# Optimization experiments

Measured on AMD Instinct MI355X. Metric: run time of the kernel, lower is better.

## Reference

```python
import jax, jax.numpy as jnp
import numpy as np

B, L, K, H = 2, 2048, 48, 128
NUM_IN = 2 * H          # h_E (H) + gathered h_V (H)
SCALE = 30.0            # EncLayer scale
LN_EPS = 1e-5


def _linear_params(key, fan_in, fan_out):
    kw, kb = jax.random.split(key)
    s = 1.0 / np.sqrt(fan_in)
    W = jax.random.uniform(kw, (fan_in, fan_out), minval=-s, maxval=s, dtype=jnp.float32)
    b = jax.random.uniform(kb, (fan_out,), minval=-s, maxval=s, dtype=jnp.float32)
    return W, b


def setup_inputs() -> dict:
    key = jax.random.key(0)
    ks = jax.random.split(key, 12)
    h_V = jax.random.normal(ks[0], (B, L, H), dtype=jnp.float32)
    h_E = jax.random.normal(ks[1], (B, L, K, H), dtype=jnp.float32)
    E_idx = jax.random.randint(ks[2], (B, L, K), 0, L, dtype=jnp.int64)
    mask_V = jnp.ones((B, L), dtype=jnp.float32)
    mask_attend = jnp.ones((B, L, K), dtype=jnp.float32)

    W1, b1 = _linear_params(ks[3], H + NUM_IN, H)
    W2, b2 = _linear_params(ks[4], H, H)
    W3, b3 = _linear_params(ks[5], H, H)
    W11, b11 = _linear_params(ks[6], H + NUM_IN, H)
    W12, b12 = _linear_params(ks[7], H, H)
    W13, b13 = _linear_params(ks[8], H, H)
    Wi, bi = _linear_params(ks[9], H, 4 * H)   # PositionWiseFeedForward W_in
    Wo, bo = _linear_params(ks[10], 4 * H, H)  # W_out

    ln = lambda: (jnp.ones((H,), jnp.float32), jnp.zeros((H,), jnp.float32))
    ln1_s, ln1_b = ln(); ln2_s, ln2_b = ln(); ln3_s, ln3_b = ln()

    return dict(h_V=h_V, h_E=h_E, E_idx=E_idx, mask_V=mask_V, mask_attend=mask_attend,
                W1=W1, b1=b1, W2=W2, b2=b2, W3=W3, b3=b3,
                W11=W11, b11=b11, W12=W12, b12=b12, W13=W13, b13=b13,
                Wi=Wi, bi=bi, Wo=Wo, bo=bo,
                ln1_s=ln1_s, ln1_b=ln1_b, ln2_s=ln2_s, ln2_b=ln2_b,
                ln3_s=ln3_s, ln3_b=ln3_b)


def gather_nodes(nodes, idx):
    # nodes: [B, L, H], idx: [B, L, K] -> [B, L, K, H]
    b, l, h = nodes.shape
    flat = idx.reshape(b, -1)  # [B, L*K]
    g = jnp.take_along_axis(nodes, flat[..., None], axis=1)  # [B, L*K, H]
    return g.reshape(b, idx.shape[1], idx.shape[2], h)


def layer_norm(x, scale, bias):
    mu = jnp.mean(x, axis=-1, keepdims=True)
    var = jnp.mean((x - mu) ** 2, axis=-1, keepdims=True)
    return (x - mu) / jnp.sqrt(var + LN_EPS) * scale + bias


def gelu(x):
    return jax.nn.gelu(x, approximate=False)  # torch nn.GELU default (erf)


def enc_layer_forward(h_V, h_E, E_idx, mask_V, mask_attend, p):
    # --- node update: gather neighbors, concat, MLP, masked sum-reduce ---
    h_EV = jnp.concatenate([h_E, gather_nodes(h_V, E_idx)], axis=-1)        # [B,L,K,2H]
    h_V_exp = jnp.broadcast_to(h_V[:, :, None, :], h_EV.shape[:3] + (h_V.shape[-1],))
    h_EV = jnp.concatenate([h_V_exp, h_EV], axis=-1)                        # [B,L,K,3H]
    m = gelu(h_EV @ p['W1'] + p['b1'])
    m = gelu(m @ p['W2'] + p['b2'])
    m = m @ p['W3'] + p['b3']
    m = mask_attend[..., None] * m
    dh = jnp.sum(m, axis=-2) / SCALE                                        # [B,L,H]
    h_V = layer_norm(h_V + dh, p['ln1_s'], p['ln1_b'])
    # --- position-wise FFN ---
    dh = gelu(h_V @ p['Wi'] + p['bi']) @ p['Wo'] + p['bo']
    h_V = layer_norm(h_V + dh, p['ln2_s'], p['ln2_b'])
    h_V = mask_V[..., None] * h_V
    # --- edge update ---
    h_EV = jnp.concatenate([h_E, gather_nodes(h_V, E_idx)], axis=-1)
    h_V_exp = jnp.broadcast_to(h_V[:, :, None, :], h_EV.shape[:3] + (h_V.shape[-1],))
    h_EV = jnp.concatenate([h_V_exp, h_EV], axis=-1)
    m = gelu(h_EV @ p['W11'] + p['b11'])
    m = gelu(m @ p['W12'] + p['b12'])
    m = m @ p['W13'] + p['b13']
    h_E = layer_norm(h_E + m, p['ln3_s'], p['ln3_b'])
    return h_V, h_E


def reference(h_V, h_E, E_idx, mask_V, mask_attend,
              W1, b1, W2, b2, W3, b3, W11, b11, W12, b12, W13, b13,
              Wi, bi, Wo, bo, ln1_s, ln1_b, ln2_s, ln2_b, ln3_s, ln3_b):
    p = dict(W1=W1, b1=b1, W2=W2, b2=b2, W3=W3, b3=b3,
             W11=W11, b11=b11, W12=W12, b12=b12, W13=W13, b13=b13,
             Wi=Wi, bi=bi, Wo=Wo, bo=bo,
             ln1_s=ln1_s, ln1_b=ln1_b, ln2_s=ln2_s, ln2_b=ln2_b,
             ln3_s=ln3_s, ln3_b=ln3_b)
    return enc_layer_forward(h_V, h_E, E_idx, mask_V, mask_attend, p)
```

## Files before the change

kernel.cpp:

```cpp
#include <hip/hip_runtime.h>
#include <hip/hip_bf16.h>
#include <math.h>

typedef unsigned short u16;
typedef __attribute__((ext_vector_type(8))) short bf16x8;
typedef __attribute__((ext_vector_type(4))) float f32x4;
typedef __attribute__((ext_vector_type(4))) unsigned int uint4v;

#define BB 2
#define LL 2048
#define KN 48
#define HH 128
#define NBLK (BB*LL)
#define ST 136

#define WOFF      16
#define OFF_W1MT  (WOFF + 0)
#define OFF_W1ST  (WOFF + 16384)
#define OFF_W1GT  (WOFF + 32768)
#define OFF_W2T   (WOFF + 49152)
#define OFF_W3T   (WOFF + 65536)
#define OFF_W11MT (WOFF + 81920)
#define OFF_W11ST (WOFF + 98304)
#define OFF_W11GT (WOFF + 114688)
#define OFF_W12T  (WOFF + 131072)
#define OFF_W13T  (WOFF + 147456)
#define OFF_WIT   (WOFF + 163840)
#define OFF_WOT   (WOFF + 229376)
#define OFF_HV1   (WOFF + 294912)
#define OFF_Q1    (WOFF + 819200)
#define OFF_Q2    (WOFF + 1343488)
#define OFF_R1    (WOFF + 1867776)
#define OFF_R2    (WOFF + 2916352)
#define PREP_N    294912

__device__ __forceinline__ float b2f(u16 u){
    union { unsigned int i; float f; } v; v.i = ((unsigned int)u) << 16; return v.f;
}
__device__ __forceinline__ u16 f2b(float f){
    unsigned int x = __float_as_uint(f);
    unsigned int r = x + 0x7fffu + ((x >> 16) & 1u);
    return (u16)(r >> 16);
}
__device__ __forceinline__ unsigned int f2b2(float lo, float hi){
    unsigned int r;
    asm("v_cvt_pk_bf16_f32 %0, %1, %2" : "=v"(r) : "v"(lo), "v"(hi));
    return r;
}
__device__ __forceinline__ float gelu_f(float x){
    float ax = fabsf(x) * 0.70710678118654752f;
    float t  = __builtin_amdgcn_rcpf(fmaf(0.3275911f, ax, 1.0f));
    float e  = __builtin_amdgcn_exp2f(ax * ax * -1.4426950408889634f);
    float p  = fmaf(1.061405429f, t, -1.453152027f);
    p = fmaf(p, t, 1.421413741f);
    p = fmaf(p, t, -0.284496736f);
    p = fmaf(p, t, 0.254829592f);
    p = p * t;
    float erfv = fmaf(-p, e, 1.0f);
    float hx = 0.5f * x;
    return fmaf(fabsf(hx), erfv, hx);
}
__device__ __forceinline__ u16 ldb(const void* p, long i, int f32){
    return f32 ? f2b(((const float*)p)[i]) : ((const u16*)p)[i];
}
__device__ __forceinline__ float ldf(const void* p, long i, int f32){
    return f32 ? ((const float*)p)[i] : b2f(((const u16*)p)[i]);
}
__device__ __forceinline__ void stage8(u16* dst, const void* src, long off, int f32){
    if (f32){
        const float* s = (const float*)src + off;
        unsigned int r0 = f2b2(s[0], s[1]);
        unsigned int r1 = f2b2(s[2], s[3]);
        unsigned int r2 = f2b2(s[4], s[5]);
        unsigned int r3 = f2b2(s[6], s[7]);
        uint4v v; v.x = r0; v.y = r1; v.z = r2; v.w = r3;
        *(uint4v*)dst = v;
    } else {
        *(uint4v*)dst = *(const uint4v*)((const u16*)src + off);
    }
}
__device__ __forceinline__ int ld_idx(const void* p, int i, int i64){
    int v = i64 ? ((const int*)p)[2*i] : ((const int*)p)[i];
    return v & (LL - 1);
}
__device__ __forceinline__ void st_out(void* p, long i, float v, int f32){
    if (f32) ((float*)p)[i] = v;
    else ((u16*)p)[i] = f2b(v);
}

__global__ void detect_kernel(const void* ln1s, const void* maskV, const void* eidx, int* flags){
    if (threadIdx.x == 0){
        unsigned l0 = ((const unsigned*)ln1s)[0];
        unsigned m0 = ((const unsigned*)maskV)[0];
        int f32 = (l0 == 0x3F800000u || m0 == 0x3F800000u) ? 1 : 0;
        const int* e = (const int*)eidx;
        int orodd = 0, orlow = 0;
        for (int i = 1; i < 64; i += 2) orodd |= e[i];
        for (int i = 0; i < 64; i += 2) orlow |= e[i];
        flags[0] = f32;
        flags[1] = (orodd == 0 && orlow != 0) ? 1 : 0;
    }
}

__global__ void prep_kernel(const void* W1, const void* W2, const void* W3,
                            const void* W11, const void* W12, const void* W13,
                            const void* Wi, const void* Wo, u16* wsbase){
    const int f32 = ((const int*)wsbase)[0];
    int i = blockIdx.x * 256 + threadIdx.x;
    if (i < 16384){ int n = i >> 7, k = i & 127; wsbase[OFF_W1MT + i] = ldb(W1, (128 + k)*128 + n, f32); }
    else if (i < 32768){ int j = i - 16384;  int n = j >> 7, k = j & 127; wsbase[OFF_W1ST  + j] = ldb(W1, k*128 + n, f32); }
    else if (i < 49152){ int j = i - 32768;  int n = j >> 7, k = j & 127; wsbase[OFF_W1GT  + j] = ldb(W1, (256 + k)*128 + n, f32); }
    else if (i < 65536){ int j = i - 49152;  int n = j >> 7, k = j & 127; wsbase[OFF_W2T   + j] = ldb(W2, k*128 + n, f32); }
    else if (i < 81920){ int j = i - 65536;  int n = j >> 7, k = j & 127; wsbase[OFF_W3T   + j] = ldb(W3, k*128 + n, f32); }
    else if (i < 98304){ int j = i - 81920;  int n = j >> 7, k = j & 127; wsbase[OFF_W11MT + j] = ldb(W11, (128 + k)*128 + n, f32); }
    else if (i < 114688){ int j = i - 98304; int n = j >> 7, k = j & 127; wsbase[OFF_W11ST + j] = ldb(W11, k*128 + n, f32); }
    else if (i < 131072){ int j = i - 114688;int n = j >> 7, k = j & 127; wsbase[OFF_W11GT + j] = ldb(W11, (256 + k)*128 + n, f32); }
    else if (i < 147456){ int j = i - 131072;int n = j >> 7, k = j & 127; wsbase[OFF_W12T  + j] = ldb(W12, k*128 + n, f32); }
    else if (i < 163840){ int j = i - 147456;int n = j >> 7, k = j & 127; wsbase[OFF_W13T  + j] = ldb(W13, k*128 + n, f32); }
    else if (i < 229376){ int j = i - 163840; int h = j >> 7, c = j & 127; wsbase[OFF_WIT + j] = ldb(Wi, c*512 + h, f32); }
    else if (i < 294912){ int j = i - 229376; int c = j >> 9, h = j & 511; wsbase[OFF_WOT + j] = ldb(Wo, h*128 + c, f32); }
}

__global__ __launch_bounds__(256) void precomp_kernel(
    const void* __restrict__ src, const void* __restrict__ bias,
    u16* __restrict__ wsbase, long offWs, long offWg, long offQ, long offR)
{
    __shared__ alignas(16) u16 X[16 * ST];
    const int f32 = ((const int*)wsbase)[0];
    const int t = threadIdx.x, lane = t & 63, w = t >> 6;
    const int node0 = blockIdx.x * 16;
    const int r16 = lane & 15, q = lane >> 4, q8 = q * 8;

    {
        int row = t >> 4, ch = t & 15;
        stage8(X + row * ST + ch * 8, src, ((long)(node0 + row)) * HH + ch * 8, f32);
    }
    __syncthreads();

    bf16x8 a[4];
    {
        const u16* ap = X + r16 * ST + q8;
#pragma unroll
        for (int kk = 0; kk < 4; kk++) a[kk] = *(const bf16x8*)(ap + kk * 32);
    }
#pragma unroll
    for (int half = 0; half < 2; half++){
        long offW = half ? offWg : offWs;
#pragma unroll
        for (int nt = 0; nt < 2; nt++){
            int col = w * 32 + nt * 16 + r16;
            const u16* bp = wsbase + offW + (long)col * 128 + q8;
            f32x4 acc; acc[0]=0.f; acc[1]=0.f; acc[2]=0.f; acc[3]=0.f;
#pragma unroll
            for (int kk = 0; kk < 4; kk++){
                bf16x8 bv = *(const bf16x8*)(bp + kk * 32);
                acc = __builtin_amdgcn_mfma_f32_16x16x32_bf16(a[kk], bv, acc, 0, 0, 0);
            }
            if (half == 0){
                float* Rf = (float*)(wsbase + offR);
                float bc = ldf(bias, col, f32);
#pragma unroll
                for (int i = 0; i < 4; i++){
                    int row = q * 4 + i;
                    Rf[(long)(node0 + row) * HH + col] = acc[i] + bc;
                }
            } else {
#pragma unroll
                for (int i = 0; i < 4; i++){
                    int row = q * 4 + i;
                    wsbase[offQ + (long)(node0 + row) * HH + col] = f2b(acc[i]);
                }
            }
        }
    }
}

__device__ __forceinline__ void mfma_regB(const u16* Als, const bf16x8* B,
                                          f32x4 acc[3], int lane){
    const int r16 = lane & 15;
    const int q8  = (lane >> 4) * 8;
    const u16* ap = Als + r16 * ST + q8;
#pragma unroll
    for (int kk = 0; kk < 4; kk++){
        bf16x8 a0 = *(const bf16x8*)(ap + kk * 32);
        bf16x8 a1 = *(const bf16x8*)(ap + 16 * ST + kk * 32);
        bf16x8 a2 = *(const bf16x8*)(ap + 32 * ST + kk * 32);
        acc[0] = __builtin_amdgcn_mfma_f32_16x16x32_bf16(a0, B[kk], acc[0], 0, 0, 0);
        acc[1] = __builtin_amdgcn_mfma_f32_16x16x32_bf16(a1, B[kk], acc[1], 0, 0, 0);
        acc[2] = __builtin_amdgcn_mfma_f32_16x16x32_bf16(a2, B[kk], acc[2], 0, 0, 0);
    }
}

__device__ __forceinline__ void zero_acc3(f32x4 acc[3]){
#pragma unroll
    for (int m = 0; m < 3; m++){ acc[m][0]=0.f; acc[m][1]=0.f; acc[m][2]=0.f; acc[m][3]=0.f; }
}

__device__ __forceinline__ void init_acc3(f32x4 acc[3], const u16* Qg, int lane, int w){
    const int r16 = lane & 15, q = lane >> 4;
    const int col = w * 16 + r16;
#pragma unroll
    for (int mt = 0; mt < 3; mt++)
#pragma unroll
        for (int i = 0; i < 4; i++){
            int r = mt * 16 + q * 4 + i;
            acc[mt][i] = b2f(Qg[r * ST + col]);
        }
}

__device__ __forceinline__ void store_m8(f32x4 acc[3], u16* M, float bc,
                                         int lane, int w, bool dogelu){
    const int r16 = lane & 15, q = lane >> 4;
    int col = w * 16 + r16;
#pragma unroll
    for (int mt = 0; mt < 3; mt++){
        float v0 = acc[mt][0] + bc, v1 = acc[mt][1] + bc;
        float v2 = acc[mt][2] + bc, v3 = acc[mt][3] + bc;
        if (dogelu){ v0 = gelu_f(v0); v1 = gelu_f(v1); v2 = gelu_f(v2); v3 = gelu_f(v3); }
        unsigned int p0 = f2b2(v0, v1), p1 = f2b2(v2, v3);
        int r = mt * 16 + q * 4;
        M[(r + 0) * ST + col] = (u16)p0;
        M[(r + 1) * ST + col] = (u16)(p0 >> 16);
        M[(r + 2) * ST + col] = (u16)p1;
        M[(r + 3) * ST + col] = (u16)(p1 >> 16);
    }
}

__global__ __launch_bounds__(512, 6) void node_kernel(
    const void* __restrict__ hV, const void* __restrict__ hE, const void* __restrict__ Eidx,
    const void* __restrict__ maskA,
    const void* __restrict__ b2, const void* __restrict__ b3,
    const void* __restrict__ ln1s, const void* __restrict__ ln1b,
    u16* __restrict__ wsbase)
{
    __shared__ alignas(16) u16 A[KN * ST];
    __shared__ alignas(16) u16 Qg[KN * ST];
    __shared__ alignas(16) u16 M1[KN * ST];
    __shared__ float smask[KN];
    __shared__ float dh[HH];
    __shared__ float hv0f[HH];
    u16* M2 = A;

    const int f32 = ((const int*)wsbase)[0];
    const int i64 = ((const int*)wsbase)[1];
    const u16* ws = wsbase;
    const int t = threadIdx.x, lane = t & 63, w = t >> 6;
    const int bid = blockIdx.x;
    const int b = bid >> 11;
    const int r16 = lane & 15, q8 = (lane >> 4) * 8;
    const int col = w * 16 + r16;

    bf16x8 B1[4];
    {
        const u16* bp = ws + OFF_W1MT + (long)col * 128 + q8;
#pragma unroll
        for (int k = 0; k < 4; k++) B1[k] = *(const bf16x8*)(bp + k * 32);
    }

    for (int i = t; i < 768; i += 512){
        int row = i >> 4, ch = i & 15;
        stage8(A + row * ST + ch * 8, hE, ((long)bid * KN + row) * HH + ch * 8, f32);
    }
    for (int i = t; i < 768; i += 512){
        int row = i >> 4, ch = i & 15;
        int nb = ld_idx(Eidx, bid * KN + row, i64);
        *(uint4v*)(Qg + row * ST + ch * 8) =
            *(const uint4v*)(ws + OFF_Q1 + ((long)b * LL + nb) * HH + ch * 8);
    }
    if (t < HH) hv0f[t] = ldf(hV, (long)bid * HH + t, f32);
    if (t < KN) smask[t] = ldf(maskA, bid * KN + t, f32);

    bf16x8 B2[4];
    {
        const u16* bp = ws + OFF_W2T + (long)col * 128 + q8;
#pragma unroll
        for (int k = 0; k < 4; k++) B2[k] = *(const bf16x8*)(bp + k * 32);
    }
    const float bcf = ((const float*)(wsbase + OFF_R1))[(long)bid * HH + col];
    __syncthreads();

    f32x4 acc[3];
    init_acc3(acc, Qg, lane, w);
    mfma_regB(A, B1, acc, lane);
    store_m8(acc, M1, bcf, lane, w, true);

    bf16x8 B3[4];
    {
        const u16* bp = ws + OFF_W3T + (long)col * 128 + q8;
#pragma unroll
        for (int k = 0; k < 4; k++) B3[k] = *(const bf16x8*)(bp + k * 32);
    }
    __syncthreads();

    zero_acc3(acc);
    mfma_regB(M1, B2, acc, lane);
    store_m8(acc, M2, ldf(b2, col, f32), lane, w, true);
    __syncthreads();

    zero_acc3(acc);
    mfma_regB(M2, B3, acc, lane);

    {
        const int q = lane >> 4;
        float bc = ldf(b3, col, f32);
        float s0 = 0.f;
#pragma unroll
        for (int mt = 0; mt < 3; mt++)
#pragma unroll
            for (int i = 0; i < 4; i++){
                int r = mt * 16 + q * 4 + i;
                s0 += smask[r] * (acc[mt][i] + bc);
            }
        s0 += __shfl_xor(s0, 16); s0 += __shfl_xor(s0, 32);
        if (lane < 16) dh[w * 16 + lane] = s0;
    }
    __syncthreads();

    if (w == 0){
        float xa = hv0f[lane]      + dh[lane]      * (1.0f / 30.0f);
        float xb = hv0f[64 + lane] + dh[64 + lane] * (1.0f / 30.0f);
        float sum = xa + xb, sq = xa * xa + xb * xb;
#pragma unroll
        for (int off = 1; off < 64; off <<= 1){ sum += __shfl_xor(sum, off); sq += __shfl_xor(sq, off); }
        float mu = sum * (1.0f / 128.0f);
        float var = sq * (1.0f / 128.0f) - mu * mu;
        float rstd = rsqrtf(var + 1e-5f);
        wsbase[OFF_HV1 + (long)bid * HH + lane] =
            f2b((xa - mu) * rstd * ldf(ln1s, lane, f32) + ldf(ln1b, lane, f32));
        wsbase[OFF_HV1 + (long)bid * HH + 64 + lane] =
            f2b((xb - mu) * rstd * ldf(ln1s, 64 + lane, f32) + ldf(ln1b, 64 + lane, f32));
    }
}

__global__ __launch_bounds__(512, 6) void ffn_kernel(
    const void* __restrict__ maskV,
    const void* __restrict__ bi, const void* __restrict__ bo,
    const void* __restrict__ ln2s, const void* __restrict__ ln2b,
    u16* __restrict__ wsbase, void* __restrict__ dout)
{
    __shared__ alignas(16) u16 X[16 * 136];
    __shared__ alignas(16) u16 Hid[16 * 520];
    __shared__ float V[16 * 132];

    const int f32 = ((const int*)wsbase)[0];
    const u16* ws = wsbase;
    const u16* hv1 = wsbase + OFF_HV1;
    const int t = threadIdx.x, lane = t & 63, w = t >> 6;
    const int node0 = blockIdx.x * 16;
    const int r16 = lane & 15, q = lane >> 4, q8 = q * 8;

    if (t < 256){
        int row = t >> 4, ch = t & 15;
        *(uint4v*)(X + row * 136 + ch * 8) =
            *(const uint4v*)(hv1 + (long)(node0 + row) * HH + ch * 8);
    }
    __syncthreads();

    bf16x8 a[4];
    {
        const u16* ap = X + r16 * 136 + q8;
#pragma unroll
        for (int kk = 0; kk < 4; kk++) a[kk] = *(const bf16x8*)(ap + kk * 32);
    }
    f32x4 acc[4];
#pragma unroll
    for (int nt = 0; nt < 4; nt++){
        acc[nt][0]=0.f; acc[nt][1]=0.f; acc[nt][2]=0.f; acc[nt][3]=0.f;
        int n = w * 64 + nt * 16 + r16;
        const u16* bp = ws + OFF_WIT + (long)n * 128 + q8;
#pragma unroll
        for (int kk = 0; kk < 4; kk++){
            bf16x8 bv = *(const bf16x8*)(bp + kk * 32);
            acc[nt] = __builtin_amdgcn_mfma_f32_16x16x32_bf16(a[kk], bv, acc[nt], 0, 0, 0);
        }
    }
#pragma unroll
    for (int nt = 0; nt < 4; nt++){
        int col = w * 64 + nt * 16 + r16;
        float bc = ldf(bi, col, f32);
        float g0 = gelu_f(acc[nt][0] + bc), g1 = gelu_f(acc[nt][1] + bc);
        float g2 = gelu_f(acc[nt][2] + bc), g3 = gelu_f(acc[nt][3] + bc);
        unsigned int p0 = f2b2(g0, g1), p1 = f2b2(g2, g3);
        int row = q * 4;
        Hid[(row + 0) * 520 + col] = (u16)p0;
        Hid[(row + 1) * 520 + col] = (u16)(p0 >> 16);
        Hid[(row + 2) * 520 + col] = (u16)p1;
        Hid[(row + 3) * 520 + col] = (u16)(p1 >> 16);
    }
    __syncthreads();

    f32x4 acc2; acc2[0]=0.f; acc2[1]=0.f; acc2[2]=0.f; acc2[3]=0.f;
    {
        const u16* ap = Hid + r16 * 520 + q8;
        const u16* bp = ws + OFF_WOT + (long)(w * 16 + r16) * 512 + q8;
#pragma unroll
        for (int kk = 0; kk < 16; kk++){
            bf16x8 av = *(const bf16x8*)(ap + kk * 32);
            bf16x8 bv = *(const bf16x8*)(bp + kk * 32);
            acc2 = __builtin_amdgcn_mfma_f32_16x16x32_bf16(av, bv, acc2, 0, 0, 0);
        }
    }
    {
        int col = w * 16 + r16;
        float bc = ldf(bo, col, f32);
#pragma unroll
        for (int i = 0; i < 4; i++){
            int row = q * 4 + i;
            V[row * 132 + col] = acc2[i] + bc + b2f(X[row * 136 + col]);
        }
    }
    __syncthreads();

    {
        int row = t >> 5, p = t & 31;
        float v0 = V[row * 132 + p * 4 + 0];
        float v1 = V[row * 132 + p * 4 + 1];
        float v2 = V[row * 132 + p * 4 + 2];
        float v3 = V[row * 132 + p * 4 + 3];
        float sum = v0 + v1 + v2 + v3;
        float sq = v0*v0 + v1*v1 + v2*v2 + v3*v3;
#pragma unroll
        for (int off = 1; off < 32; off <<= 1){ sum += __shfl_xor(sum, off); sq += __shfl_xor(sq, off); }
        float mu = sum * (1.0f / 128.0f);
        float var = sq * (1.0f / 128.0f) - mu * mu;
        float rstd = rsqrtf(var + 1e-5f);
        float mv = ldf(maskV, node0 + row, f32);
        long base = (long)(node0 + row) * HH;
#pragma unroll
        for (int j = 0; j < 4; j++){
            int c = p * 4 + j;
            float v = (j==0)?v0:(j==1)?v1:(j==2)?v2:v3;
            float y = ((v - mu) * rstd * ldf(ln2s, c, f32) + ldf(ln2b, c, f32)) * mv;
            st_out(dout, base + c, y, f32);
        }
    }
}

__global__ __launch_bounds__(512, 6) void edge_kernel(
    const void* __restrict__ hE, const void* __restrict__ Eidx,
    const void* __restrict__ b12, const void* __restrict__ b13,
    const void* __restrict__ ln3s, const void* __restrict__ ln3b,
    u16* __restrict__ wsbase, void* __restrict__ dout)
{
    __shared__ alignas(16) u16 A[KN * ST];
    __shared__ alignas(16) u16 Qg[KN * ST];
    __shared__ alignas(16) u16 M1[KN * ST];
    __shared__ float rowsum[KN];
    __shared__ float rowsq[KN];
    u16* M2 = A;

    const int f32 = ((const int*)wsbase)[0];
    const int i64 = ((const int*)wsbase)[1];
    const u16* ws = wsbase;
    const int t = threadIdx.x, lane = t & 63, w = t >> 6;
    const int bid = blockIdx.x;
    const int b = bid >> 11;
    const int r16 = lane & 15, q8 = (lane >> 4) * 8;
    const int col = w * 16 + r16;

    bf16x8 B1[4];
    {
        const u16* bp = ws + OFF_W11MT + (long)col * 128 + q8;
#pragma unroll
        for (int k = 0; k < 4; k++) B1[k] = *(const bf16x8*)(bp + k * 32);
    }

    for (int i = t; i < 768; i += 512){
        int row = i >> 4, ch = i & 15;
        stage8(A + row * ST + ch * 8, hE, ((long)bid * KN + row) * HH + ch * 8, f32);
    }
    for (int i = t; i < 768; i += 512){
        int row = i >> 4, ch = i & 15;
        int nb = ld_idx(Eidx, bid * KN + row, i64);
        *(uint4v*)(Qg + row * ST + ch * 8) =
            *(const uint4v*)(ws + OFF_Q2 + ((long)b * LL + nb) * HH + ch * 8);
    }
    if (t < KN){ rowsum[t] = 0.f; rowsq[t] = 0.f; }

    bf16x8 B2[4];
    {
        const u16* bp = ws + OFF_W12T + (long)col * 128 + q8;
#pragma unroll
        for (int k = 0; k < 4; k++) B2[k] = *(const bf16x8*)(bp + k * 32);
    }
    const float bcf = ((const float*)(wsbase + OFF_R2))[(long)bid * HH + col];
    __syncthreads();

    f32x4 acc[3];
    init_acc3(acc, Qg, lane, w);
    mfma_regB(A, B1, acc, lane);
    store_m8(acc, M1, bcf, lane, w, true);

    bf16x8 B3[4];
    {
        const u16* bp = ws + OFF_W13T + (long)col * 128 + q8;
#pragma unroll
        for (int k = 0; k < 4; k++) B3[k] = *(const bf16x8*)(bp + k * 32);
    }
    __syncthreads();

    zero_acc3(acc);
    mfma_regB(M1, B2, acc, lane);
    store_m8(acc, M2, ldf(b12, col, f32), lane, w, true);
    __syncthreads();

    zero_acc3(acc);
    mfma_regB(M2, B3, acc, lane);

    const int q = lane >> 4;
    float vals[3][4];
    {
        float bc = ldf(b13, col, f32);
#pragma unroll
        for (int mt = 0; mt < 3; mt++)
#pragma unroll
            for (int i = 0; i < 4; i++){
                int r = mt * 16 + q * 4 + i;
                vals[mt][i] = acc[mt][i] + bc + ldf(hE, ((long)bid * KN + r) * HH + col, f32);
            }
    }
#pragma unroll
    for (int mt = 0; mt < 3; mt++)
#pragma unroll
        for (int i = 0; i < 4; i++){
            float s = vals[mt][i], sq2 = vals[mt][i] * vals[mt][i];
            s += __shfl_xor(s, 1); sq2 += __shfl_xor(sq2, 1);
            s += __shfl_xor(s, 2); sq2 += __shfl_xor(sq2, 2);
            s += __shfl_xor(s, 4); sq2 += __shfl_xor(sq2, 4);
            s += __shfl_xor(s, 8); sq2 += __shfl_xor(sq2, 8);
            if (r16 == 0){
                int r = mt * 16 + q * 4 + i;
                atomicAdd(&rowsum[r], s);
                atomicAdd(&rowsq[r], sq2);
            }
        }
    __syncthreads();
    if (t < KN){
        float mu = rowsum[t] * (1.0f / 128.0f);
        float var = rowsq[t] * (1.0f / 128.0f) - mu * mu;
        rowsum[t] = mu;
        rowsq[t] = rsqrtf(var + 1e-5f);
    }
    __syncthreads();

    {
        long ebase = (long)BB * LL * HH;
        float g = ldf(ln3s, col, f32), be = ldf(ln3b, col, f32);
#pragma unroll
        for (int mt = 0; mt < 3; mt++)
#pragma unroll
            for (int i = 0; i < 4; i++){
                int r = mt * 16 + q * 4 + i;
                long base = ebase + ((long)bid * KN + r) * HH;
                st_out(dout, base + col, (vals[mt][i] - rowsum[r]) * rowsq[r] * g + be, f32);
            }
    }
}

extern "C" void kernel_launch(void* const* d_in, const int* in_sizes, int n_in,
                              void* d_out, int out_size, void* d_ws, size_t ws_size,
                              hipStream_t stream) {
    const void* hV    = d_in[0];
    const void* hE    = d_in[1];
    const void* Eidx  = d_in[2];
    const void* maskV = d_in[3];
    const void* maskA = d_in[4];
    const void* W1  = d_in[5];  const void* b1  = d_in[6];
    const void* W2  = d_in[7];  const void* b2  = d_in[8];
    const void* W3  = d_in[9];  const void* b3  = d_in[10];
    const void* W11 = d_in[11]; const void* b11 = d_in[12];
    const void* W12 = d_in[13]; const void* b12 = d_in[14];
    const void* W13 = d_in[15]; const void* b13 = d_in[16];
    const void* Wi  = d_in[17]; const void* bi  = d_in[18];
    const void* Wo  = d_in[19]; const void* bo  = d_in[20];
    const void* ln1s = d_in[21]; const void* ln1b = d_in[22];
    const void* ln2s = d_in[23]; const void* ln2b = d_in[24];
    const void* ln3s = d_in[25]; const void* ln3b = d_in[26];

    u16* ws = (u16*)d_ws;

    detect_kernel<<<1, 64, 0, stream>>>(ln1s, maskV, Eidx, (int*)d_ws);
    prep_kernel<<<(PREP_N + 255) / 256, 256, 0, stream>>>(W1, W2, W3, W11, W12, W13, Wi, Wo, ws);
    precomp_kernel<<<NBLK / 16, 256, 0, stream>>>(hV, b1, ws,
                                                  (long)OFF_W1ST, (long)OFF_W1GT,
                                                  (long)OFF_Q1, (long)OFF_R1);
    node_kernel<<<NBLK, 512, 0, stream>>>(hV, hE, Eidx, maskA,
                                          b2, b3, ln1s, ln1b, ws);
    ffn_kernel<<<NBLK / 16, 512, 0, stream>>>(maskV, bi, bo, ln2s, ln2b, ws, d_out);
    precomp_kernel<<<NBLK / 16, 256, 0, stream>>>(d_out, b11, ws,
                                                  (long)OFF_W11ST, (long)OFF_W11GT,
                                                  (long)OFF_Q2, (long)OFF_R2);
    edge_kernel<<<NBLK, 512, 0, stream>>>(hE, Eidx, b12, b13,
                                          ln3s, ln3b, ws, d_out);
}
```

Measured before the change: 378.3 us.

## Transpose MFMA operand roles for vectorized stores and fuse precomp into FFN

Swaps the A/B operands of all MFMAs so weights become the row operand. Each lane then holds four contiguous output columns, which lets bias loads, LDS stores, residual loads and output stores use 4-wide vector accesses instead of scalar strided ones. The second precomp launch is folded into the end of the FFN kernel, which computes the W11 self/gather projections from the just-normalized h_V kept in LDS and saves a launch and a reread of the output. It also sets s_setprio around the MFMA loops and simplifies the LayerNorm reductions to use fewer shuffles.

```diff
diff --git a/kernel.cpp b/kernel.cpp
--- a/kernel.cpp
+++ b/kernel.cpp
@@ -6,6 +6,8 @@
 typedef __attribute__((ext_vector_type(8))) short bf16x8;
 typedef __attribute__((ext_vector_type(4))) float f32x4;
 typedef __attribute__((ext_vector_type(4))) unsigned int uint4v;
+typedef __attribute__((ext_vector_type(2))) unsigned int uint2v;
+typedef __attribute__((ext_vector_type(4))) unsigned short u16x4;
 
 #define BB 2
 #define LL 2048
@@ -66,14 +68,32 @@
 __device__ __forceinline__ float ldf(const void* p, long i, int f32){
     return f32 ? ((const float*)p)[i] : b2f(((const u16*)p)[i]);
 }
+__device__ __forceinline__ f32x4 ldf4(const void* p, long i, int f32){
+    f32x4 r;
+    if (f32){
+        r = *(const f32x4*)((const float*)p + i);
+    } else {
+        u16x4 v = *(const u16x4*)((const u16*)p + i);
+        r[0]=b2f(v[0]); r[1]=b2f(v[1]); r[2]=b2f(v[2]); r[3]=b2f(v[3]);
+    }
+    return r;
+}
+__device__ __forceinline__ void st4(void* p, long i, f32x4 v, int f32){
+    if (f32){
+        *(f32x4*)((float*)p + i) = v;
+    } else {
+        uint2v u; u.x = f2b2(v[0], v[1]); u.y = f2b2(v[2], v[3]);
+        *(uint2v*)((u16*)p + i) = u;
+    }
+}
 __device__ __forceinline__ void stage8(u16* dst, const void* src, long off, int f32){
     if (f32){
         const float* s = (const float*)src + off;
-        unsigned int r0 = f2b2(s[0], s[1]);
-        unsigned int r1 = f2b2(s[2], s[3]);
-        unsigned int r2 = f2b2(s[4], s[5]);
-        unsigned int r3 = f2b2(s[6], s[7]);
-        uint4v v; v.x = r0; v.y = r1; v.z = r2; v.w = r3;
+        f32x4 a = *(const f32x4*)(s);
+        f32x4 b = *(const f32x4*)(s + 4);
+        uint4v v;
+        v.x = f2b2(a[0], a[1]); v.y = f2b2(a[2], a[3]);
+        v.z = f2b2(b[0], b[1]); v.w = f2b2(b[2], b[3]);
         *(uint4v*)dst = v;
     } else {
         *(uint4v*)dst = *(const uint4v*)((const u16*)src + off);
@@ -82,10 +102,6 @@
 __device__ __forceinline__ int ld_idx(const void* p, int i, int i64){
     int v = i64 ? ((const int*)p)[2*i] : ((const int*)p)[i];
     return v & (LL - 1);
-}
-__device__ __forceinline__ void st_out(void* p, long i, float v, int f32){
-    if (f32) ((float*)p)[i] = v;
-    else ((u16*)p)[i] = f2b(v);
 }
 
 __global__ void detect_kernel(const void* ln1s, const void* maskV, const void* eidx, int* flags){
@@ -137,57 +153,48 @@
     }
     __syncthreads();
 
-    bf16x8 a[4];
-    {
-        const u16* ap = X + r16 * ST + q8;
-#pragma unroll
-        for (int kk = 0; kk < 4; kk++) a[kk] = *(const bf16x8*)(ap + kk * 32);
-    }
+    const u16* bp = X + r16 * ST + q8;
 #pragma unroll
     for (int half = 0; half < 2; half++){
         long offW = half ? offWg : offWs;
 #pragma unroll
         for (int nt = 0; nt < 2; nt++){
-            int col = w * 32 + nt * 16 + r16;
-            const u16* bp = wsbase + offW + (long)col * 128 + q8;
+            int wr = w * 32 + nt * 16 + r16;
+            const u16* ap = wsbase + offW + (long)wr * 128 + q8;
             f32x4 acc; acc[0]=0.f; acc[1]=0.f; acc[2]=0.f; acc[3]=0.f;
 #pragma unroll
             for (int kk = 0; kk < 4; kk++){
+                bf16x8 av = *(const bf16x8*)(ap + kk * 32);
                 bf16x8 bv = *(const bf16x8*)(bp + kk * 32);
-                acc = __builtin_amdgcn_mfma_f32_16x16x32_bf16(a[kk], bv, acc, 0, 0, 0);
+                acc = __builtin_amdgcn_mfma_f32_16x16x32_bf16(av, bv, acc, 0, 0, 0);
             }
+            int c0 = w * 32 + nt * 16 + q * 4;
             if (half == 0){
+                f32x4 bc = ldf4(bias, c0, f32);
                 float* Rf = (float*)(wsbase + offR);
-                float bc = ldf(bias, col, f32);
-#pragma unroll
-                for (int i = 0; i < 4; i++){
-                    int row = q * 4 + i;
-                    Rf[(long)(node0 + row) * HH + col] = acc[i] + bc;
-                }
+                f32x4 rr; rr[0]=acc[0]+bc[0]; rr[1]=acc[1]+bc[1]; rr[2]=acc[2]+bc[2]; rr[3]=acc[3]+bc[3];
+                *(f32x4*)(Rf + (long)(node0 + r16) * HH + c0) = rr;
             } else {
-#pragma unroll
-                for (int i = 0; i < 4; i++){
-                    int row = q * 4 + i;
-                    wsbase[offQ + (long)(node0 + row) * HH + col] = f2b(acc[i]);
-                }
+                uint2v u; u.x = f2b2(acc[0], acc[1]); u.y = f2b2(acc[2], acc[3]);
+                *(uint2v*)(wsbase + offQ + (long)(node0 + r16) * HH + c0) = u;
             }
         }
     }
 }
 
-__device__ __forceinline__ void mfma_regB(const u16* Als, const bf16x8* B,
-                                          f32x4 acc[3], int lane){
+__device__ __forceinline__ void mfma_WB(const u16* Mls, const bf16x8* W,
+                                        f32x4 acc[3], int lane){
     const int r16 = lane & 15;
     const int q8  = (lane >> 4) * 8;
-    const u16* ap = Als + r16 * ST + q8;
+    const u16* bp = Mls + r16 * ST + q8;
 #pragma unroll
     for (int kk = 0; kk < 4; kk++){
-        bf16x8 a0 = *(const bf16x8*)(ap + kk * 32);
-        bf16x8 a1 = *(const bf16x8*)(ap + 16 * ST + kk * 32);
-        bf16x8 a2 = *(const bf16x8*)(ap + 32 * ST + kk * 32);
-        acc[0] = __builtin_amdgcn_mfma_f32_16x16x32_bf16(a0, B[kk], acc[0], 0, 0, 0);
-        acc[1] = __builtin_amdgcn_mfma_f32_16x16x32_bf16(a1, B[kk], acc[1], 0, 0, 0);
-        acc[2] = __builtin_amdgcn_mfma_f32_16x16x32_bf16(a2, B[kk], acc[2], 0, 0, 0);
+        bf16x8 b0 = *(const bf16x8*)(bp + kk * 32);
+        bf16x8 b1 = *(const bf16x8*)(bp + 16 * ST + kk * 32);
+        bf16x8 b2 = *(const bf16x8*)(bp + 32 * ST + kk * 32);
+        acc[0] = __builtin_amdgcn_mfma_f32_16x16x32_bf16(W[kk], b0, acc[0], 0, 0, 0);
+        acc[1] = __builtin_amdgcn_mfma_f32_16x16x32_bf16(W[kk], b1, acc[1], 0, 0, 0);
+        acc[2] = __builtin_amdgcn_mfma_f32_16x16x32_bf16(W[kk], b2, acc[2], 0, 0, 0);
     }
 }
 
@@ -196,33 +203,27 @@
     for (int m = 0; m < 3; m++){ acc[m][0]=0.f; acc[m][1]=0.f; acc[m][2]=0.f; acc[m][3]=0.f; }
 }
 
-__device__ __forceinline__ void init_acc3(f32x4 acc[3], const u16* Qg, int lane, int w){
+__device__ __forceinline__ void init_accT(f32x4 acc[3], const u16* Qg, int lane, int w){
     const int r16 = lane & 15, q = lane >> 4;
-    const int col = w * 16 + r16;
-#pragma unroll
-    for (int mt = 0; mt < 3; mt++)
-#pragma unroll
-        for (int i = 0; i < 4; i++){
-            int r = mt * 16 + q * 4 + i;
-            acc[mt][i] = b2f(Qg[r * ST + col]);
-        }
-}
-
-__device__ __forceinline__ void store_m8(f32x4 acc[3], u16* M, float bc,
-                                         int lane, int w, bool dogelu){
+    const int c0 = w * 16 + q * 4;
+#pragma unroll
+    for (int mt = 0; mt < 3; mt++){
+        u16x4 v = *(const u16x4*)(Qg + (mt * 16 + r16) * ST + c0);
+        acc[mt][0]=b2f(v[0]); acc[mt][1]=b2f(v[1]); acc[mt][2]=b2f(v[2]); acc[mt][3]=b2f(v[3]);
+    }
+}
+
+__device__ __forceinline__ void store_T(f32x4 acc[3], u16* M, f32x4 bc4,
+                                        int lane, int w, bool dogelu){
     const int r16 = lane & 15, q = lane >> 4;
-    int col = w * 16 + r16;
+    const int c0 = w * 16 + q * 4;
 #pragma unroll
     for (int mt = 0; mt < 3; mt++){
-        float v0 = acc[mt][0] + bc, v1 = acc[mt][1] + bc;
-        float v2 = acc[mt][2] + bc, v3 = acc[mt][3] + bc;
+        float v0 = acc[mt][0] + bc4[0], v1 = acc[mt][1] + bc4[1];
+        float v2 = acc[mt][2] + bc4[2], v3 = acc[mt][3] + bc4[3];
         if (dogelu){ v0 = gelu_f(v0); v1 = gelu_f(v1); v2 = gelu_f(v2); v3 = gelu_f(v3); }
-        unsigned int p0 = f2b2(v0, v1), p1 = f2b2(v2, v3);
-        int r = mt * 16 + q * 4;
-        M[(r + 0) * ST + col] = (u16)p0;
-        M[(r + 1) * ST + col] = (u16)(p0 >> 16);
-        M[(r + 2) * ST + col] = (u16)p1;
-        M[(r + 3) * ST + col] = (u16)(p1 >> 16);
+        uint2v u; u.x = f2b2(v0, v1); u.y = f2b2(v2, v3);
+        *(uint2v*)(M + (mt * 16 + r16) * ST + c0) = u;
     }
 }
 
@@ -237,7 +238,7 @@
     __shared__ alignas(16) u16 Qg[KN * ST];
     __shared__ alignas(16) u16 M1[KN * ST];
     __shared__ float smask[KN];
-    __shared__ float dh[HH];
+    __shared__ alignas(16) float dh[HH];
     __shared__ float hv0f[HH];
     u16* M2 = A;
 
@@ -247,12 +248,13 @@
     const int t = threadIdx.x, lane = t & 63, w = t >> 6;
     const int bid = blockIdx.x;
     const int b = bid >> 11;
-    const int r16 = lane & 15, q8 = (lane >> 4) * 8;
-    const int col = w * 16 + r16;
+    const int r16 = lane & 15, q = lane >> 4, q8 = q * 8;
+    const int wrow = w * 16 + r16;
+    const int c0 = w * 16 + q * 4;
 
     bf16x8 B1[4];
     {
-        const u16* bp = ws + OFF_W1MT + (long)col * 128 + q8;
+        const u16* bp = ws + OFF_W1MT + (long)wrow * 128 + q8;
 #pragma unroll
         for (int k = 0; k < 4; k++) B1[k] = *(const bf16x8*)(bp + k * 32);
     }
@@ -272,47 +274,55 @@
 
     bf16x8 B2[4];
     {
-        const u16* bp = ws + OFF_W2T + (long)col * 128 + q8;
+        const u16* bp = ws + OFF_W2T + (long)wrow * 128 + q8;
 #pragma unroll
         for (int k = 0; k < 4; k++) B2[k] = *(const bf16x8*)(bp + k * 32);
     }
-    const float bcf = ((const float*)(wsbase + OFF_R1))[(long)bid * HH + col];
+    const f32x4 bc1 = *(const f32x4*)((const float*)(wsbase + OFF_R1) + (long)bid * HH + c0);
     __syncthreads();
 
     f32x4 acc[3];
-    init_acc3(acc, Qg, lane, w);
-    mfma_regB(A, B1, acc, lane);
-    store_m8(acc, M1, bcf, lane, w, true);
+    init_accT(acc, Qg, lane, w);
+    __builtin_amdgcn_s_setprio(1);
+    mfma_WB(A, B1, acc, lane);
+    __builtin_amdgcn_s_setprio(0);
+    store_T(acc, M1, bc1, lane, w, true);
 
     bf16x8 B3[4];
     {
-        const u16* bp = ws + OFF_W3T + (long)col * 128 + q8;
+        const u16* bp = ws + OFF_W3T + (long)wrow * 128 + q8;
 #pragma unroll
         for (int k = 0; k < 4; k++) B3[k] = *(const bf16x8*)(bp + k * 32);
     }
     __syncthreads();
 
     zero_acc3(acc);
-    mfma_regB(M1, B2, acc, lane);
-    store_m8(acc, M2, ldf(b2, col, f32), lane, w, true);
+    __builtin_amdgcn_s_setprio(1);
+    mfma_WB(M1, B2, acc, lane);
+    __builtin_amdgcn_s_setprio(0);
+    store_T(acc, M2, ldf4(b2, c0, f32), lane, w, true);
     __syncthreads();
 
     zero_acc3(acc);
-    mfma_regB(M2, B3, acc, lane);
-
-    {
-        const int q = lane >> 4;
-        float bc = ldf(b3, col, f32);
-        float s0 = 0.f;
-#pragma unroll
-        for (int mt = 0; mt < 3; mt++)
-#pragma unroll
-            for (int i = 0; i < 4; i++){
-                int r = mt * 16 + q * 4 + i;
-                s0 += smask[r] * (acc[mt][i] + bc);
-            }
-        s0 += __shfl_xor(s0, 16); s0 += __shfl_xor(s0, 32);
-        if (lane < 16) dh[w * 16 + lane] = s0;
+    __builtin_amdgcn_s_setprio(1);
+    mfma_WB(M2, B3, acc, lane);
+    __builtin_amdgcn_s_setprio(0);
+
+    {
+        f32x4 b3v = ldf4(b3, c0, f32);
+        f32x4 s; s[0]=0.f; s[1]=0.f; s[2]=0.f; s[3]=0.f;
+#pragma unroll
+        for (int mt = 0; mt < 3; mt++){
+            float mk = smask[mt * 16 + r16];
+#pragma unroll
+            for (int j = 0; j < 4; j++) s[j] += mk * (acc[mt][j] + b3v[j]);
+        }
+#pragma unroll
+        for (int off = 1; off <= 8; off <<= 1){
+#pragma unroll
+            for (int j = 0; j < 4; j++) s[j] += __shfl_xor(s[j], off);
+        }
+        if (r16 == 0) *(f32x4*)&dh[c0] = s;
     }
     __syncthreads();
 
@@ -335,12 +345,13 @@
 __global__ __launch_bounds__(512, 6) void ffn_kernel(
     const void* __restrict__ maskV,
     const void* __restrict__ bi, const void* __restrict__ bo,
+    const void* __restrict__ b11,
     const void* __restrict__ ln2s, const void* __restrict__ ln2b,
     u16* __restrict__ wsbase, void* __restrict__ dout)
 {
     __shared__ alignas(16) u16 X[16 * 136];
     __shared__ alignas(16) u16 Hid[16 * 520];
-    __shared__ float V[16 * 132];
+    __shared__ alignas(16) float V[16 * 132];
 
     const int f32 = ((const int*)wsbase)[0];
     const u16* ws = wsbase;
@@ -348,6 +359,7 @@
     const int t = threadIdx.x, lane = t & 63, w = t >> 6;
     const int node0 = blockIdx.x * 16;
     const int r16 = lane & 15, q = lane >> 4, q8 = q * 8;
+    const int c0 = w * 16 + q * 4;
 
     if (t < 256){
         int row = t >> 4, ch = t & 15;
@@ -356,83 +368,100 @@
     }
     __syncthreads();
 
-    bf16x8 a[4];
-    {
-        const u16* ap = X + r16 * 136 + q8;
-#pragma unroll
-        for (int kk = 0; kk < 4; kk++) a[kk] = *(const bf16x8*)(ap + kk * 32);
-    }
     f32x4 acc[4];
 #pragma unroll
-    for (int nt = 0; nt < 4; nt++){
-        acc[nt][0]=0.f; acc[nt][1]=0.f; acc[nt][2]=0.f; acc[nt][3]=0.f;
-        int n = w * 64 + nt * 16 + r16;
-        const u16* bp = ws + OFF_WIT + (long)n * 128 + q8;
+    for (int nt = 0; nt < 4; nt++){ acc[nt][0]=0.f; acc[nt][1]=0.f; acc[nt][2]=0.f; acc[nt][3]=0.f; }
+    {
+        const u16* bp = X + r16 * 136 + q8;
 #pragma unroll
         for (int kk = 0; kk < 4; kk++){
             bf16x8 bv = *(const bf16x8*)(bp + kk * 32);
-            acc[nt] = __builtin_amdgcn_mfma_f32_16x16x32_bf16(a[kk], bv, acc[nt], 0, 0, 0);
+#pragma unroll
+            for (int nt = 0; nt < 4; nt++){
+                const u16* ap = ws + OFF_WIT + (long)(w * 64 + nt * 16 + r16) * 128 + kk * 32 + q8;
+                bf16x8 av = *(const bf16x8*)ap;
+                acc[nt] = __builtin_amdgcn_mfma_f32_16x16x32_bf16(av, bv, acc[nt], 0, 0, 0);
+            }
         }
     }
 #pragma unroll
     for (int nt = 0; nt < 4; nt++){
-        int col = w * 64 + nt * 16 + r16;
-        float bc = ldf(bi, col, f32);
-        float g0 = gelu_f(acc[nt][0] + bc), g1 = gelu_f(acc[nt][1] + bc);
-        float g2 = gelu_f(acc[nt][2] + bc), g3 = gelu_f(acc[nt][3] + bc);
-        unsigned int p0 = f2b2(g0, g1), p1 = f2b2(g2, g3);
-        int row = q * 4;
-        Hid[(row + 0) * 520 + col] = (u16)p0;
-        Hid[(row + 1) * 520 + col] = (u16)(p0 >> 16);
-        Hid[(row + 2) * 520 + col] = (u16)p1;
-        Hid[(row + 3) * 520 + col] = (u16)(p1 >> 16);
+        int hc0 = w * 64 + nt * 16 + q * 4;
+        f32x4 bc = ldf4(bi, hc0, f32);
+        float g0 = gelu_f(acc[nt][0] + bc[0]), g1 = gelu_f(acc[nt][1] + bc[1]);
+        float g2 = gelu_f(acc[nt][2] + bc[2]), g3 = gelu_f(acc[nt][3] + bc[3]);
+        uint2v u; u.x = f2b2(g0, g1); u.y = f2b2(g2, g3);
+        *(uint2v*)(Hid + r16 * 520 + hc0) = u;
     }
     __syncthreads();
 
     f32x4 acc2; acc2[0]=0.f; acc2[1]=0.f; acc2[2]=0.f; acc2[3]=0.f;
     {
-        const u16* ap = Hid + r16 * 520 + q8;
-        const u16* bp = ws + OFF_WOT + (long)(w * 16 + r16) * 512 + q8;
+        const u16* ap = ws + OFF_WOT + (long)(w * 16 + r16) * 512 + q8;
+        const u16* bp = Hid + r16 * 520 + q8;
+        __builtin_amdgcn_s_setprio(1);
 #pragma unroll
         for (int kk = 0; kk < 16; kk++){
             bf16x8 av = *(const bf16x8*)(ap + kk * 32);
             bf16x8 bv = *(const bf16x8*)(bp + kk * 32);
             acc2 = __builtin_amdgcn_mfma_f32_16x16x32_bf16(av, bv, acc2, 0, 0, 0);
         }
-    }
-    {
-        int col = w * 16 + r16;
-        float bc = ldf(bo, col, f32);
-#pragma unroll
-        for (int i = 0; i < 4; i++){
-            int row = q * 4 + i;
-            V[row * 132 + col] = acc2[i] + bc + b2f(X[row * 136 + col]);
-        }
+        __builtin_amdgcn_s_setprio(0);
+    }
+    {
+        f32x4 bo4 = ldf4(bo, c0, f32);
+        u16x4 xr = *(const u16x4*)(X + r16 * 136 + c0);
+        f32x4 vv;
+        vv[0] = acc2[0] + bo4[0] + b2f(xr[0]);
+        vv[1] = acc2[1] + bo4[1] + b2f(xr[1]);
+        vv[2] = acc2[2] + bo4[2] + b2f(xr[2]);
+        vv[3] = acc2[3] + bo4[3] + b2f(xr[3]);
+        *(f32x4*)&V[r16 * 132 + c0] = vv;
     }
     __syncthreads();
 
     {
         int row = t >> 5, p = t & 31;
-        float v0 = V[row * 132 + p * 4 + 0];
-        float v1 = V[row * 132 + p * 4 + 1];
-        float v2 = V[row * 132 + p * 4 + 2];
-        float v3 = V[row * 132 + p * 4 + 3];
-        float sum = v0 + v1 + v2 + v3;
-        float sq = v0*v0 + v1*v1 + v2*v2 + v3*v3;
+        f32x4 v = *(const f32x4*)&V[row * 132 + p * 4];
+        float sum = v[0] + v[1] + v[2] + v[3];
+        float sq = v[0]*v[0] + v[1]*v[1] + v[2]*v[2] + v[3]*v[3];
 #pragma unroll
         for (int off = 1; off < 32; off <<= 1){ sum += __shfl_xor(sum, off); sq += __shfl_xor(sq, off); }
         float mu = sum * (1.0f / 128.0f);
         float var = sq * (1.0f / 128.0f) - mu * mu;
         float rstd = rsqrtf(var + 1e-5f);
         float mv = ldf(maskV, node0 + row, f32);
-        long base = (long)(node0 + row) * HH;
-#pragma unroll
-        for (int j = 0; j < 4; j++){
-            int c = p * 4 + j;
-            float v = (j==0)?v0:(j==1)?v1:(j==2)?v2:v3;
-            float y = ((v - mu) * rstd * ldf(ln2s, c, f32) + ldf(ln2b, c, f32)) * mv;
-            st_out(dout, base + c, y, f32);
-        }
+        f32x4 s4 = ldf4(ln2s, p * 4, f32), bb4 = ldf4(ln2b, p * 4, f32);
+        f32x4 y;
+#pragma unroll
+        for (int j = 0; j < 4; j++) y[j] = ((v[j] - mu) * rstd * s4[j] + bb4[j]) * mv;
+        st4(dout, (long)(node0 + row) * HH + p * 4, y, f32);
+        uint2v u; u.x = f2b2(y[0], y[1]); u.y = f2b2(y[2], y[3]);
+        *(uint2v*)(X + row * 136 + p * 4) = u;
+    }
+    __syncthreads();
+
+    {
+        const u16* bp = X + r16 * 136 + q8;
+        f32x4 aR, aQ;
+        aR[0]=0.f; aR[1]=0.f; aR[2]=0.f; aR[3]=0.f;
+        aQ[0]=0.f; aQ[1]=0.f; aQ[2]=0.f; aQ[3]=0.f;
+#pragma unroll
+        for (int kk = 0; kk < 4; kk++){
+            bf16x8 bv = *(const bf16x8*)(bp + kk * 32);
+            bf16x8 avR = *(const bf16x8*)(ws + OFF_W11ST + (long)(w * 16 + r16) * 128 + kk * 32 + q8);
+            bf16x8 avQ = *(const bf16x8*)(ws + OFF_W11GT + (long)(w * 16 + r16) * 128 + kk * 32 + q8);
+            aR = __builtin_amdgcn_mfma_f32_16x16x32_bf16(avR, bv, aR, 0, 0, 0);
+            aQ = __builtin_amdgcn_mfma_f32_16x16x32_bf16(avQ, bv, aQ, 0, 0, 0);
+        }
+        f32x4 b11v = ldf4(b11, c0, f32);
+        float* Rf = (float*)(wsbase + OFF_R2);
+        f32x4 rr;
+#pragma unroll
+        for (int j = 0; j < 4; j++) rr[j] = aR[j] + b11v[j];
+        *(f32x4*)(Rf + (long)(node0 + r16) * HH + c0) = rr;
+        uint2v u; u.x = f2b2(aQ[0], aQ[1]); u.y = f2b2(aQ[2], aQ[3]);
+        *(uint2v*)(wsbase + OFF_Q2 + (long)(node0 + r16) * HH + c0) = u;
     }
 }
 
@@ -455,12 +484,13 @@
     const int t = threadIdx.x, lane = t & 63, w = t >> 6;
     const int bid = blockIdx.x;
     const int b = bid >> 11;
-    const int r16 = lane & 15, q8 = (lane >> 4) * 8;
-    const int col = w * 16 + r16;
+    const int r16 = lane & 15, q = lane >> 4, q8 = q * 8;
+    const int wrow = w * 16 + r16;
+    const int c0 = w * 16 + q * 4;
 
     bf16x8 B1[4];
     {
-        const u16* bp = ws + OFF_W11MT + (long)col * 128 + q8;
+        const u16* bp = ws + OFF_W11MT + (long)wrow * 128 + q8;
 #pragma unroll
         for (int k = 0; k < 4; k++) B1[k] = *(const bf16x8*)(bp + k * 32);
     }
@@ -479,61 +509,69 @@
 
     bf16x8 B2[4];
     {
-        const u16* bp = ws + OFF_W12T + (long)col * 128 + q8;
+        const u16* bp = ws + OFF_W12T + (long)wrow * 128 + q8;
 #pragma unroll
         for (int k = 0; k < 4; k++) B2[k] = *(const bf16x8*)(bp + k * 32);
     }
-    const float bcf = ((const float*)(wsbase + OFF_R2))[(long)bid * HH + col];
+    const f32x4 bc1 = *(const f32x4*)((const float*)(wsbase + OFF_R2) + (long)bid * HH + c0);
     __syncthreads();
 
     f32x4 acc[3];
-    init_acc3(acc, Qg, lane, w);
-    mfma_regB(A, B1, acc, lane);
-    store_m8(acc, M1, bcf, lane, w, true);
+    init_accT(acc, Qg, lane, w);
+    __builtin_amdgcn_s_setprio(1);
+    mfma_WB(A, B1, acc, lane);
+    __builtin_amdgcn_s_setprio(0);
+    store_T(acc, M1, bc1, lane, w, true);
 
     bf16x8 B3[4];
     {
-        const u16* bp = ws + OFF_W13T + (long)col * 128 + q8;
+        const u16* bp = ws + OFF_W13T + (long)wrow * 128 + q8;
 #pragma unroll
         for (int k = 0; k < 4; k++) B3[k] = *(const bf16x8*)(bp + k * 32);
     }
     __syncthreads();
 
     zero_acc3(acc);
-    mfma_regB(M1, B2, acc, lane);
-    store_m8(acc, M2, ldf(b12, col, f32), lane, w, true);
+    __builtin_amdgcn_s_setprio(1);
+    mfma_WB(M1, B2, acc, lane);
+    __builtin_amdgcn_s_setprio(0);
+    store_T(acc, M2, ldf4(b12, c0, f32), lane, w, true);
     __syncthreads();
 
     zero_acc3(acc);
-    mfma_regB(M2, B3, acc, lane);
-
-    const int q = lane >> 4;
-    float vals[3][4];
-    {
-        float bc = ldf(b13, col, f32);
-#pragma unroll
-        for (int mt = 0; mt < 3; mt++)
-#pragma unroll
-            for (int i = 0; i < 4; i++){
-                int r = mt * 16 + q * 4 + i;
-                vals[mt][i] = acc[mt][i] + bc + ldf(hE, ((long)bid * KN + r) * HH + col, f32);
+    __builtin_amdgcn_s_setprio(1);
+    mfma_WB(M2, B3, acc, lane);
+    __builtin_amdgcn_s_setprio(0);
+
+    f32x4 vals[3];
+    {
+        f32x4 b13v = ldf4(b13, c0, f32);
+#pragma unroll
+        for (int mt = 0; mt < 3; mt++){
+            int r = mt * 16 + r16;
+            f32x4 res = ldf4(hE, ((long)bid * KN + r) * HH + c0, f32);
+#pragma unroll
+            for (int j = 0; j < 4; j++) vals[mt][j] = acc[mt][j] + b13v[j] + res[j];
+        }
+    }
+    {
+        float s[3], ss[3];
+#pragma unroll
+        for (int mt = 0; mt < 3; mt++){
+            s[mt]  = vals[mt][0] + vals[mt][1] + vals[mt][2] + vals[mt][3];
+            ss[mt] = vals[mt][0]*vals[mt][0] + vals[mt][1]*vals[mt][1]
+                   + vals[mt][2]*vals[mt][2] + vals[mt][3]*vals[mt][3];
+            s[mt]  += __shfl_xor(s[mt], 16);  s[mt]  += __shfl_xor(s[mt], 32);
+            ss[mt] += __shfl_xor(ss[mt], 16); ss[mt] += __shfl_xor(ss[mt], 32);
+        }
+        if (lane < 16){
+#pragma unroll
+            for (int mt = 0; mt < 3; mt++){
+                atomicAdd(&rowsum[mt * 16 + lane], s[mt]);
+                atomicAdd(&rowsq[mt * 16 + lane], ss[mt]);
             }
-    }
-#pragma unroll
-    for (int mt = 0; mt < 3; mt++)
-#pragma unroll
-        for (int i = 0; i < 4; i++){
-            float s = vals[mt][i], sq2 = vals[mt][i] * vals[mt][i];
-            s += __shfl_xor(s, 1); sq2 += __shfl_xor(sq2, 1);
-            s += __shfl_xor(s, 2); sq2 += __shfl_xor(sq2, 2);
-            s += __shfl_xor(s, 4); sq2 += __shfl_xor(sq2, 4);
-            s += __shfl_xor(s, 8); sq2 += __shfl_xor(sq2, 8);
-            if (r16 == 0){
-                int r = mt * 16 + q * 4 + i;
-                atomicAdd(&rowsum[r], s);
-                atomicAdd(&rowsq[r], sq2);
-            }
-        }
+        }
+    }
     __syncthreads();
     if (t < KN){
         float mu = rowsum[t] * (1.0f / 128.0f);
@@ -545,15 +583,16 @@
 
     {
         long ebase = (long)BB * LL * HH;
-        float g = ldf(ln3s, col, f32), be = ldf(ln3b, col, f32);
-#pragma unroll
-        for (int mt = 0; mt < 3; mt++)
-#pragma unroll
-            for (int i = 0; i < 4; i++){
-                int r = mt * 16 + q * 4 + i;
-                long base = ebase + ((long)bid * KN + r) * HH;
-                st_out(dout, base + col, (vals[mt][i] - rowsum[r]) * rowsq[r] * g + be, f32);
-            }
+        f32x4 g4 = ldf4(ln3s, c0, f32), be4 = ldf4(ln3b, c0, f32);
+#pragma unroll
+        for (int mt = 0; mt < 3; mt++){
+            int r = mt * 16 + r16;
+            float mu = rowsum[r], rs = rowsq[r];
+            f32x4 y;
+#pragma unroll
+            for (int j = 0; j < 4; j++) y[j] = (vals[mt][j] - mu) * rs * g4[j] + be4[j];
+            st4(dout, ebase + ((long)bid * KN + r) * HH + c0, y, f32);
+        }
     }
 }
 
@@ -586,10 +625,7 @@
                                                   (long)OFF_Q1, (long)OFF_R1);
     node_kernel<<<NBLK, 512, 0, stream>>>(hV, hE, Eidx, maskA,
                                           b2, b3, ln1s, ln1b, ws);
-    ffn_kernel<<<NBLK / 16, 512, 0, stream>>>(maskV, bi, bo, ln2s, ln2b, ws, d_out);
-    precomp_kernel<<<NBLK / 16, 256, 0, stream>>>(d_out, b11, ws,
-                                                  (long)OFF_W11ST, (long)OFF_W11GT,
-                                                  (long)OFF_Q2, (long)OFF_R2);
+    ffn_kernel<<<NBLK / 16, 512, 0, stream>>>(maskV, bi, bo, b11, ln2s, ln2b, ws, d_out);
     edge_kernel<<<NBLK, 512, 0, stream>>>(hE, Eidx, b12, b13,
                                           ln3s, ln3b, ws, d_out);
 }
```

New measurement: 373.1 us. No clear change (-1.4%).
